# Performance work log

Hardware: AMD Instinct MI355X
Metric: run time of the kernel (lower is better)

Reference implementation:

```python
import jax, jax.numpy as jnp
import numpy as np
import math

B, L, DIM = 128, 192, 512
NTOKEN = 100
MAX_BONDS = 6
MAX_LEN = 192


def _sinusoidal_pe(max_len, dim):
    pos = np.arange(max_len, dtype=np.float32)[:, None]
    div = np.exp(np.arange(0, dim, 2, dtype=np.float32) * (-math.log(10000.0) / dim))
    pe = np.zeros((max_len, dim), dtype=np.float32)
    pe[:, 0::2] = np.sin(pos * div)
    pe[:, 1::2] = np.cos(pos * div)
    return jnp.asarray(pe[:, None, :])  # [max_len, 1, dim]


def setup_inputs() -> dict:
    key = jax.random.key(0)
    ks = jax.random.split(key, 16)
    s = 0.02
    inp = {
        "element": jax.random.randint(ks[0], (B, L), 0, NTOKEN),
        "bond": jax.random.randint(ks[1], (B, L, MAX_BONDS), 0, L),
        "aroma": jax.random.randint(ks[2], (B, L), 0, 2),
        "charge": jax.random.randint(ks[3], (B, L), 0, 6),
        "segment": jax.random.randint(ks[4], (B, L), 0, 30),
        # parameters
        "pe": _sinusoidal_pe(MAX_LEN, DIM),
        "E_elem": jax.random.normal(ks[5], (NTOKEN, DIM), jnp.float32) * s,
        "E_charge": jax.random.normal(ks[6], (13, DIM), jnp.float32) * s,
        "E_aroma": jax.random.normal(ks[7], (2, DIM), jnp.float32) * s,
        "E_seg": jax.random.normal(ks[8], (30, DIM), jnp.float32) * s,
        "W1": jax.random.normal(ks[9], (DIM, 4 * DIM), jnp.float32) * s,
        "b1": jnp.zeros((4 * DIM,), jnp.float32),
        "W2": jax.random.normal(ks[10], (4 * DIM, DIM), jnp.float32) * s,
        "b2": jnp.zeros((DIM,), jnp.float32),
        "W3": jax.random.normal(ks[11], (DIM, 4 * DIM), jnp.float32) * s,
        "b3": jnp.zeros((4 * DIM,), jnp.float32),
        "W4": jax.random.normal(ks[12], (4 * DIM, DIM), jnp.float32) * s,
        "b4": jnp.zeros((DIM,), jnp.float32),
        "W5": jax.random.normal(ks[13], (DIM, DIM), jnp.float32) * s,
        "b5": jnp.zeros((DIM,), jnp.float32),
    }
    return inp


def _mlp(x, W1, b1, W2, b2, W3, b3, W4, b4, W5, b5):
    x = x + jnp.maximum(x @ W1 + b1, 0.0) @ W2 + b2
    x = x + jnp.maximum(x @ W3 + b3, 0.0) @ W4 + b4
    return x @ W5 + b5


def reference(element, bond, aroma, charge, segment, pe,
              E_elem, E_charge, E_aroma, E_seg,
              W1, b1, W2, b2, W3, b3, W4, b4, W5, b5):
    b, l = element.shape
    # embeddings: all [l, b, dim]
    emb = E_elem[element.T]
    emb = emb + pe[:l]                      # [l,1,dim] broadcast (eval: dropout off)
    emb = emb + E_aroma[aroma.T]
    emb = emb + E_charge[charge.T + 6]
    emb = emb + E_seg[segment.T]
    message = _mlp(emb, W1, b1, W2, b2, W3, b3, W4, b4, W5, b5)  # [l,b,dim]
    # bond aggregation: agg[k] = sum_m message[bond[b,k,m]] excluding self-bonds
    # (equivalent to the dense one-hot einsum with the diagonal masked out)
    msg_bld = jnp.transpose(message, (1, 0, 2))          # [b,l,dim]
    g = msg_bld[jnp.arange(b)[:, None, None], bond]      # [b,l,MAX_BONDS,dim]
    mask = (bond != jnp.arange(l)[None, :, None]).astype(message.dtype)
    agg = jnp.einsum('bkmd,bkm->bkd', g, mask)           # [b,l,dim]
    return emb + jnp.transpose(agg, (1, 0, 2))           # [l,b,dim]
```

## Files before the change

### kernel.cpp

```cpp
#include <hip/hip_runtime.h>
#include <cstdint>
#include <cstddef>

typedef unsigned short u16;
typedef unsigned int u32;

typedef unsigned short u16x8 __attribute__((ext_vector_type(8)));
typedef __bf16 bf16x8 __attribute__((ext_vector_type(8)));
typedef float f32x4 __attribute__((ext_vector_type(4)));
typedef float f32x8 __attribute__((ext_vector_type(8)));

#define NB   128
#define NL   192
#define NTOK (NB * NL)
#define DIM  512
#define HID  2048

static __device__ __forceinline__ float bf2f(u16 h) {
    union { u32 u; float f; } v; v.u = ((u32)h) << 16; return v.f;
}
static __device__ __forceinline__ u16 f2bf(float f) {
    union { float f; u32 u; } v; v.f = f;
    u32 u = v.u + 0x7FFF + ((v.u >> 16) & 1);
    return (u16)(u >> 16);
}

__global__ void transpose_f2b(const float* __restrict__ in, u16* __restrict__ out,
                              int K, int N) {
    __shared__ float tile[32][33];
    int tx = threadIdx.x & 31, ty = threadIdx.x >> 5;
    int n0 = blockIdx.x * 32, k0 = blockIdx.y * 32;
#pragma unroll
    for (int i = 0; i < 4; i++)
        tile[ty + i * 8][tx] = in[(size_t)(k0 + ty + i * 8) * N + n0 + tx];
    __syncthreads();
#pragma unroll
    for (int i = 0; i < 4; i++)
        out[(size_t)(n0 + ty + i * 8) * K + k0 + tx] = f2bf(tile[tx][ty + i * 8]);
}

static __device__ __forceinline__ void add8f(float* acc, const float* p) {
    f32x8 v = *(const f32x8*)p;
#pragma unroll
    for (int i = 0; i < 8; i++) acc[i] += v[i];
}

__global__ void embed_kernel(const int* __restrict__ element, const int* __restrict__ aroma,
                             const int* __restrict__ charge, const int* __restrict__ segment,
                             const float* __restrict__ pe, const float* __restrict__ E_elem,
                             const float* __restrict__ E_charge, const float* __restrict__ E_aroma,
                             const float* __restrict__ E_seg,
                             float* __restrict__ emb32, u16* __restrict__ emb16) {
    int t = blockIdx.x * 4 + (threadIdx.x >> 6);
    int lane = threadIdx.x & 63;
    int l = t >> 7, b = t & 127;
    int d = lane * 8;
    int idx = b * NL + l;
    int e = element[idx];
    int a = aroma[idx];
    int c = charge[idx] + 6;
    int s = segment[idx];
    float acc[8] = {0, 0, 0, 0, 0, 0, 0, 0};
    add8f(acc, E_elem  + (size_t)e * DIM + d);
    add8f(acc, pe      + (size_t)l * DIM + d);
    add8f(acc, E_aroma + (size_t)a * DIM + d);
    add8f(acc, E_charge+ (size_t)c * DIM + d);
    add8f(acc, E_seg   + (size_t)s * DIM + d);
    f32x8 o32; u16x8 o16;
#pragma unroll
    for (int i = 0; i < 8; i++) { o32[i] = acc[i]; o16[i] = f2bf(acc[i]); }
    *(f32x8*)(emb32 + (size_t)t * DIM + d) = o32;
    *(u16x8*)(emb16 + (size_t)t * DIM + d) = o16;
}

__global__ __launch_bounds__(256, 2) void gemm_bt(
    const u16* __restrict__ A, const u16* __restrict__ BT,
    const float* __restrict__ bias, const u16* __restrict__ resid16,
    const float* __restrict__ resid32,
    u16* __restrict__ C, int M, int N, int K, int do_relu) {
    __shared__ __align__(16) u16 As[3][128 * 32];
    __shared__ __align__(16) u16 Bs[3][256 * 32];

    const int tid  = threadIdx.x;
    const int wave = tid >> 6;
    const int lane = tid & 63;
    const int m0 = blockIdx.x * 128;
    const int n0 = blockIdx.y * 256;
    const int wm = (wave >> 1) * 64;
    const int wn = (wave & 1) * 128;
    const int lr = lane >> 2;
    const int lc = (lane & 3) * 8;
    const int fr = lane & 15;
    const int fq = lane >> 4;

    f32x4 acc[4][8] = {};

    const u16* Ag0 = A  + (size_t)(m0 + wave * 16 + lr) * K + lc;
    const u16* Ag1 = Ag0 + (size_t)64 * K;
    const u16* Bg0 = BT + (size_t)(n0 + wave * 16 + lr) * K + lc;
    const u16* Bg1 = Bg0 + (size_t)64 * K;
    const u16* Bg2 = Bg0 + (size_t)128 * K;
    const u16* Bg3 = Bg0 + (size_t)192 * K;
    const int sA0 = (wave * 16) * 32;
    const int sA1 = (64 + wave * 16) * 32;
    const int sB0 = (wave * 16) * 32;
    const int sB1 = (64 + wave * 16) * 32;
    const int sB2 = (128 + wave * 16) * 32;
    const int sB3 = (192 + wave * 16) * 32;

#define GLL(gp, lp) __builtin_amdgcn_global_load_lds(                            \
        (const __attribute__((address_space(1))) void*)(gp),                     \
        (__attribute__((address_space(3))) void*)(lp), 16, 0, 0)
#define STAGE(buf, k0) do {                                                      \
    GLL(Ag0 + (k0), &As[buf][sA0]);                                              \
    GLL(Ag1 + (k0), &As[buf][sA1]);                                              \
    GLL(Bg0 + (k0), &Bs[buf][sB0]);                                              \
    GLL(Bg1 + (k0), &Bs[buf][sB1]);                                              \
    GLL(Bg2 + (k0), &Bs[buf][sB2]);                                              \
    GLL(Bg3 + (k0), &Bs[buf][sB3]);                                              \
} while (0)

    const int kIters = K >> 5;
    STAGE(0, 0);
    STAGE(1, 32);
    STAGE(2, 64);

    int cur = 0;
    for (int k = 0; k < kIters; ++k) {
        asm volatile("s_waitcnt vmcnt(12)\n\ts_barrier" ::: "memory");

        bf16x8 af[4], bg[8];
#pragma unroll
        for (int i = 0; i < 4; i++)
            af[i] = *(const bf16x8*)(&As[cur][(wm + i * 16 + fr) * 32 + fq * 8]);
#pragma unroll
        for (int j = 0; j < 8; j++)
            bg[j] = *(const bf16x8*)(&Bs[cur][(wn + j * 16 + fr) * 32 + fq * 8]);
#pragma unroll
        for (int i = 0; i < 4; i++)
#pragma unroll
            for (int j = 0; j < 8; j++)
                acc[i][j] = __builtin_amdgcn_mfma_f32_16x16x32_bf16(
                    af[i], bg[j], acc[i][j], 0, 0, 0);

        asm volatile("s_barrier" ::: "memory");
        const int knext = (k + 3 < kIters) ? (k + 3) << 5 : 0;
        STAGE(cur, knext);
        cur = (cur == 2) ? 0 : cur + 1;
    }
#undef STAGE
#undef GLL

#pragma unroll
    for (int j = 0; j < 8; j++) {
        int n = n0 + wn + j * 16 + fr;
        float bv = bias[n];
#pragma unroll
        for (int i = 0; i < 4; i++) {
#pragma unroll
            for (int r = 0; r < 4; r++) {
                int m = m0 + wm + i * 16 + fq * 4 + r;
                float v = acc[i][j][r] + bv;
                if (do_relu) v = fmaxf(v, 0.0f);
                if (resid16) v += bf2f(resid16[(size_t)m * N + n]);
                if (resid32) v += resid32[(size_t)m * N + n];
                C[(size_t)m * N + n] = f2bf(v);
            }
        }
    }
}

__global__ void agg_kernel(const float* __restrict__ emb32, const u16* __restrict__ msg,
                           const int* __restrict__ bond, float* __restrict__ out) {
    int t = blockIdx.x * 4 + (threadIdx.x >> 6);
    int lane = threadIdx.x & 63;
    int l = t >> 7, b = t & 127;
    int d = lane * 8;
    float acc[8];
    {
        f32x8 v = *(const f32x8*)(emb32 + (size_t)t * DIM + d);
#pragma unroll
        for (int i = 0; i < 8; i++) acc[i] = v[i];
    }
    const int* bp = bond + ((size_t)b * NL + l) * 6;
#pragma unroll
    for (int m = 0; m < 6; m++) {
        int j = bp[m];
        if (j != l) {
            u16x8 g = *(const u16x8*)(msg + ((size_t)j * NB + b) * DIM + d);
#pragma unroll
            for (int i = 0; i < 8; i++) acc[i] += bf2f(g[i]);
        }
    }
    f32x8 o;
#pragma unroll
    for (int i = 0; i < 8; i++) o[i] = acc[i];
    *(f32x8*)(out + (size_t)t * DIM + d) = o;
}

extern "C" void kernel_launch(void* const* d_in, const int* in_sizes, int n_in,
                              void* d_out, int out_size, void* d_ws, size_t ws_size,
                              hipStream_t stream) {
    const int* element = (const int*)d_in[0];
    const int* bond    = (const int*)d_in[1];
    const int* aroma   = (const int*)d_in[2];
    const int* charge  = (const int*)d_in[3];
    const int* segment = (const int*)d_in[4];
    const float* pe      = (const float*)d_in[5];
    const float* E_elem  = (const float*)d_in[6];
    const float* E_charge= (const float*)d_in[7];
    const float* E_aroma = (const float*)d_in[8];
    const float* E_seg   = (const float*)d_in[9];
    const float* W1 = (const float*)d_in[10];
    const float* b1 = (const float*)d_in[11];
    const float* W2 = (const float*)d_in[12];
    const float* b2 = (const float*)d_in[13];
    const float* W3 = (const float*)d_in[14];
    const float* b3 = (const float*)d_in[15];
    const float* W4 = (const float*)d_in[16];
    const float* b4 = (const float*)d_in[17];
    const float* W5 = (const float*)d_in[18];
    const float* b5 = (const float*)d_in[19];

    float* emb32 = (float*)d_out;

    char* ws = (char*)d_ws;
    size_t woff = 0;
    auto take = [&](size_t bytes) -> u16* {
        u16* p = (u16*)(ws + woff);
        woff += (bytes + 255) & ~(size_t)255;
        return p;
    };
    u16* W1T = take((size_t)HID * DIM * 2);
    u16* W2T = take((size_t)DIM * HID * 2);
    u16* W3T = take((size_t)HID * DIM * 2);
    u16* W4T = take((size_t)DIM * HID * 2);
    u16* W5T = take((size_t)DIM * DIM * 2);
    u16* emb16 = take((size_t)NTOK * DIM * 2);
    u16* msg   = take((size_t)NTOK * DIM * 2);

    static const int ncs[] = {1, 2, 3, 4, 6, 8, 12, 16, 24, 32, 48, 64, 96, 192};
    int CM = 128;
    for (int nc : ncs) {
        int cm = NTOK / nc;
        size_t need = woff + ((size_t)cm * HID * 2 + 256)
                           + ((size_t)cm * DIM * 2 + 256) * 2;
        if (need <= ws_size) { CM = cm; break; }
    }
    u16* hC  = take((size_t)CM * HID * 2);
    u16* xaC = take((size_t)CM * DIM * 2);
    u16* xbC = take((size_t)CM * DIM * 2);

    transpose_f2b<<<dim3(HID / 32, DIM / 32), 256, 0, stream>>>(W1, W1T, DIM, HID);
    transpose_f2b<<<dim3(DIM / 32, HID / 32), 256, 0, stream>>>(W2, W2T, HID, DIM);
    transpose_f2b<<<dim3(HID / 32, DIM / 32), 256, 0, stream>>>(W3, W3T, DIM, HID);
    transpose_f2b<<<dim3(DIM / 32, HID / 32), 256, 0, stream>>>(W4, W4T, HID, DIM);
    transpose_f2b<<<dim3(DIM / 32, DIM / 32), 256, 0, stream>>>(W5, W5T, DIM, DIM);

    embed_kernel<<<NTOK / 4, 256, 0, stream>>>(element, aroma, charge, segment, pe,
                                               E_elem, E_charge, E_aroma, E_seg,
                                               emb32, emb16);

    for (int c0 = 0; c0 < NTOK; c0 += CM) {
        const u16* x16 = emb16 + (size_t)c0 * DIM;
        const float* x32 = emb32 + (size_t)c0 * DIM;
        u16* msgC = msg + (size_t)c0 * DIM;
        gemm_bt<<<dim3(CM / 128, HID / 256), 256, 0, stream>>>(x16, W1T, b1, nullptr, nullptr, hC,  CM, HID, DIM, 1);
        gemm_bt<<<dim3(CM / 128, DIM / 256), 256, 0, stream>>>(hC,  W2T, b2, nullptr, x32,     xaC, CM, DIM, HID, 0);
        gemm_bt<<<dim3(CM / 128, HID / 256), 256, 0, stream>>>(xaC, W3T, b3, nullptr, nullptr, hC,  CM, HID, DIM, 1);
        gemm_bt<<<dim3(CM / 128, DIM / 256), 256, 0, stream>>>(hC,  W4T, b4, xaC,    nullptr,  xbC, CM, DIM, HID, 0);
        gemm_bt<<<dim3(CM / 128, DIM / 256), 256, 0, stream>>>(xbC, W5T, b5, nullptr, nullptr, msgC, CM, DIM, DIM, 0);
    }

    agg_kernel<<<NTOK / 4, 256, 0, stream>>>(emb32, msg, bond, (float*)d_out);
}
```

Measured before the change: 562.8 us.

## Swizzle LDS layout, remap workgroups, stage epilogue through LDS, trim pipeline tail

Reworks the GEMM kernel in several ways at once. It XOR-swizzles the LDS column index to cut bank conflicts on fragment reads and remaps the 1D workgroup id across XCD-strided groups for better L2 locality. It raises wave priority around the MFMA block and drops redundant tail loads by tightening vmcnt waits near the end of K. The epilogue now writes through LDS so each row gets coalesced 16-byte global stores, at the cost of extra barriers and LDS traffic.

Result: faster. 517.4 us (-8.1%).

```diff
diff --git a/kernel.cpp b/kernel.cpp
--- a/kernel.cpp
+++ b/kernel.cpp
@@ -78,20 +78,28 @@
     const float* __restrict__ bias, const u16* __restrict__ resid16,
     const float* __restrict__ resid32,
     u16* __restrict__ C, int M, int N, int K, int do_relu) {
-    __shared__ __align__(16) u16 As[3][128 * 32];
-    __shared__ __align__(16) u16 Bs[3][256 * 32];
+    __shared__ __align__(16) u16 smem[3 * 128 * 32 + 3 * 256 * 32];
+    u16* As = smem;
+    u16* Bs = smem + 3 * 128 * 32;
 
     const int tid  = threadIdx.x;
     const int wave = tid >> 6;
     const int lane = tid & 63;
-    const int m0 = blockIdx.x * 128;
-    const int n0 = blockIdx.y * 256;
+
+    const int nwg = gridDim.x;
+    const int bid = blockIdx.x;
+    const int wg  = ((nwg & 7) == 0) ? ((bid & 7) * (nwg >> 3) + (bid >> 3)) : bid;
+    const int nt  = N >> 8;
+    const int m0  = (wg / nt) * 128;
+    const int n0  = (wg % nt) * 256;
+
     const int wm = (wave >> 1) * 64;
     const int wn = (wave & 1) * 128;
     const int lr = lane >> 2;
-    const int lc = (lane & 3) * 8;
+    const int lc = (((lane & 3) ^ ((lr >> 1) & 3)) * 8);
     const int fr = lane & 15;
     const int fq = lane >> 4;
+    const int fc = ((fq ^ ((fr >> 1) & 3)) * 8);
 
     f32x4 acc[4][8] = {};
 
@@ -112,12 +120,12 @@
         (const __attribute__((address_space(1))) void*)(gp),                     \
         (__attribute__((address_space(3))) void*)(lp), 16, 0, 0)
 #define STAGE(buf, k0) do {                                                      \
-    GLL(Ag0 + (k0), &As[buf][sA0]);                                              \
-    GLL(Ag1 + (k0), &As[buf][sA1]);                                              \
-    GLL(Bg0 + (k0), &Bs[buf][sB0]);                                              \
-    GLL(Bg1 + (k0), &Bs[buf][sB1]);                                              \
-    GLL(Bg2 + (k0), &Bs[buf][sB2]);                                              \
-    GLL(Bg3 + (k0), &Bs[buf][sB3]);                                              \
+    GLL(Ag0 + (k0), &As[(buf) * 4096 + sA0]);                                    \
+    GLL(Ag1 + (k0), &As[(buf) * 4096 + sA1]);                                    \
+    GLL(Bg0 + (k0), &Bs[(buf) * 8192 + sB0]);                                    \
+    GLL(Bg1 + (k0), &Bs[(buf) * 8192 + sB1]);                                    \
+    GLL(Bg2 + (k0), &Bs[(buf) * 8192 + sB2]);                                    \
+    GLL(Bg3 + (k0), &Bs[(buf) * 8192 + sB3]);                                    \
 } while (0)
 
     const int kIters = K >> 5;
@@ -127,30 +135,43 @@
 
     int cur = 0;
     for (int k = 0; k < kIters; ++k) {
-        asm volatile("s_waitcnt vmcnt(12)\n\ts_barrier" ::: "memory");
-
+        if (k + 2 < kIters)
+            asm volatile("s_waitcnt vmcnt(12)\n\ts_barrier" ::: "memory");
+        else if (k + 2 == kIters)
+            asm volatile("s_waitcnt vmcnt(6)\n\ts_barrier" ::: "memory");
+        else
+            asm volatile("s_waitcnt vmcnt(0)\n\ts_barrier" ::: "memory");
+
+        const u16* Ab = &As[cur * 4096];
+        const u16* Bb = &Bs[cur * 8192];
         bf16x8 af[4], bg[8];
 #pragma unroll
         for (int i = 0; i < 4; i++)
-            af[i] = *(const bf16x8*)(&As[cur][(wm + i * 16 + fr) * 32 + fq * 8]);
+            af[i] = *(const bf16x8*)(&Ab[(wm + i * 16 + fr) * 32 + fc]);
 #pragma unroll
         for (int j = 0; j < 8; j++)
-            bg[j] = *(const bf16x8*)(&Bs[cur][(wn + j * 16 + fr) * 32 + fq * 8]);
+            bg[j] = *(const bf16x8*)(&Bb[(wn + j * 16 + fr) * 32 + fc]);
+
+        __builtin_amdgcn_s_setprio(1);
 #pragma unroll
         for (int i = 0; i < 4; i++)
 #pragma unroll
             for (int j = 0; j < 8; j++)
                 acc[i][j] = __builtin_amdgcn_mfma_f32_16x16x32_bf16(
                     af[i], bg[j], acc[i][j], 0, 0, 0);
-
-        asm volatile("s_barrier" ::: "memory");
-        const int knext = (k + 3 < kIters) ? (k + 3) << 5 : 0;
-        STAGE(cur, knext);
+        __builtin_amdgcn_s_setprio(0);
+
+        if (k + 3 < kIters) {
+            asm volatile("s_barrier" ::: "memory");
+            STAGE(cur, (k + 3) << 5);
+        }
         cur = (cur == 2) ? 0 : cur + 1;
     }
 #undef STAGE
 #undef GLL
 
+    __syncthreads();
+#define CSTR 264
 #pragma unroll
     for (int j = 0; j < 8; j++) {
         int n = n0 + wn + j * 16 + fr;
@@ -164,10 +185,22 @@
                 if (do_relu) v = fmaxf(v, 0.0f);
                 if (resid16) v += bf2f(resid16[(size_t)m * N + n]);
                 if (resid32) v += resid32[(size_t)m * N + n];
-                C[(size_t)m * N + n] = f2bf(v);
+                smem[(wm + i * 16 + fq * 4 + r) * CSTR + wn + j * 16 + fr] = f2bf(v);
             }
         }
     }
+    __syncthreads();
+    {
+        const int erow = tid >> 5;
+        const int ecol = (tid & 31) * 8;
+#pragma unroll
+        for (int rr = 0; rr < 16; ++rr) {
+            int row = rr * 8 + erow;
+            *(u16x8*)(C + (size_t)(m0 + row) * N + n0 + ecol) =
+                *(const u16x8*)(&smem[row * CSTR + ecol]);
+        }
+    }
+#undef CSTR
 }
 
 __global__ void agg_kernel(const float* __restrict__ emb32, const u16* __restrict__ msg,
@@ -265,11 +298,12 @@
         const u16* x16 = emb16 + (size_t)c0 * DIM;
         const float* x32 = emb32 + (size_t)c0 * DIM;
         u16* msgC = msg + (size_t)c0 * DIM;
-        gemm_bt<<<dim3(CM / 128, HID / 256), 256, 0, stream>>>(x16, W1T, b1, nullptr, nullptr, hC,  CM, HID, DIM, 1);
-        gemm_bt<<<dim3(CM / 128, DIM / 256), 256, 0, stream>>>(hC,  W2T, b2, nullptr, x32,     xaC, CM, DIM, HID, 0);
-        gemm_bt<<<dim3(CM / 128, HID / 256), 256, 0, stream>>>(xaC, W3T, b3, nullptr, nullptr, hC,  CM, HID, DIM, 1);
-        gemm_bt<<<dim3(CM / 128, DIM / 256), 256, 0, stream>>>(hC,  W4T, b4, xaC,    nullptr,  xbC, CM, DIM, HID, 0);
-        gemm_bt<<<dim3(CM / 128, DIM / 256), 256, 0, stream>>>(xbC, W5T, b5, nullptr, nullptr, msgC, CM, DIM, DIM, 0);
+        int mt = CM / 128;
+        gemm_bt<<<dim3(mt * (HID / 256)), 256, 0, stream>>>(x16, W1T, b1, nullptr, nullptr, hC,  CM, HID, DIM, 1);
+        gemm_bt<<<dim3(mt * (DIM / 256)), 256, 0, stream>>>(hC,  W2T, b2, nullptr, x32,     xaC, CM, DIM, HID, 0);
+        gemm_bt<<<dim3(mt * (HID / 256)), 256, 0, stream>>>(xaC, W3T, b3, nullptr, nullptr, hC,  CM, HID, DIM, 1);
+        gemm_bt<<<dim3(mt * (DIM / 256)), 256, 0, stream>>>(hC,  W4T, b4, xaC,    nullptr,  xbC, CM, DIM, HID, 0);
+        gemm_bt<<<dim3(mt * (DIM / 256)), 256, 0, stream>>>(xbC, W5T, b5, nullptr, nullptr, msgC, CM, DIM, DIM, 0);
     }
 
     agg_kernel<<<NTOK / 4, 256, 0, stream>>>(emb32, msg, bond, (float*)d_out);
```
